# Performance work log

Measured on AMD Instinct MI355X. Metric: run time of the kernel, lower is better.

Reference implementation:

```python
import jax, jax.numpy as jnp
import numpy as np

N, IN_DIM, HID, Z, HEADS, E = 10000, 128, 128, 64, 4, 320000
NEG_SLOPE = 0.2


def setup_inputs() -> dict:
    key = jax.random.key(0)
    ks = jax.random.split(key, 16)
    s = 0.1
    return {
        "x": jax.random.normal(ks[0], (N, IN_DIM), jnp.float32),
        "edge_index": jax.random.randint(ks[1], (2, E), 0, N, jnp.int64),
        "gcn_w": jax.random.normal(ks[2], (IN_DIM, HID), jnp.float32) * s,
        "gcn_b": jnp.zeros((HID,), jnp.float32),
        "gat_w": jax.random.normal(ks[3], (HID, HEADS * HID), jnp.float32) * s,
        "gat_att_src": jax.random.normal(ks[4], (HEADS, HID), jnp.float32) * s,
        "gat_att_dst": jax.random.normal(ks[5], (HEADS, HID), jnp.float32) * s,
        "gat_b": jnp.zeros((HID,), jnp.float32),
        "mlp_w1": jax.random.normal(ks[6], (HID, HID), jnp.float32) * s,
        "mlp_b1": jnp.zeros((HID,), jnp.float32),
        "mlp_w2": jax.random.normal(ks[7], (HID, HID), jnp.float32) * s,
        "mlp_b2": jnp.zeros((HID,), jnp.float32),
        "mu_w": jax.random.normal(ks[8], (HID, Z), jnp.float32) * s,
        "mu_b": jnp.zeros((Z,), jnp.float32),
        "lv_w": jax.random.normal(ks[9], (HID, Z), jnp.float32) * s,
        "lv_b": jnp.zeros((Z,), jnp.float32),
    }


def _add_self_loops(edge_index, n):
    loop = jnp.arange(n, dtype=edge_index.dtype)
    src = jnp.concatenate([edge_index[0], loop])
    dst = jnp.concatenate([edge_index[1], loop])
    return src, dst


def _gcn(x, edge_index, w, b):
    # PyG GCNConv: add self-loops, symmetric normalization D^-1/2 (A+I) D^-1/2
    n = x.shape[0]
    src, dst = _add_self_loops(edge_index, n)
    deg = jax.ops.segment_sum(jnp.ones_like(dst, dtype=x.dtype), dst, num_segments=n)
    dinv = jax.lax.rsqrt(deg)  # deg >= 1 due to self-loops
    norm = dinv[src] * dinv[dst]  # [E+N]
    h = x @ w  # [N, HID]
    out = jax.ops.segment_sum(h[src] * norm[:, None], dst, num_segments=n)
    return out + b


def _gat(x, edge_index, w, att_src, att_dst, b):
    # PyG GATConv(heads=HEADS, concat=False): average heads, self-loops added
    n = x.shape[0]
    src, dst = _add_self_loops(edge_index, n)
    h = (x @ w).reshape(n, HEADS, HID)  # [N, H, C]
    a_src = jnp.einsum('nhc,hc->nh', h, att_src)  # [N, H]
    a_dst = jnp.einsum('nhc,hc->nh', h, att_dst)
    e = jax.nn.leaky_relu(a_src[src] + a_dst[dst], NEG_SLOPE)  # [E+N, H]
    # segment softmax over incoming edges of each destination node
    emax = jax.ops.segment_max(e, dst, num_segments=n)
    e = jnp.exp(e - emax[dst])
    denom = jax.ops.segment_sum(e, dst, num_segments=n)
    alpha = e / denom[dst]  # [E+N, H]
    out = jax.ops.segment_sum(h[src] * alpha[:, :, None], dst, num_segments=n)  # [N, H, C]
    return out.mean(axis=1) + b


def reference(x, edge_index, gcn_w, gcn_b, gat_w, gat_att_src, gat_att_dst, gat_b,
              mlp_w1, mlp_b1, mlp_w2, mlp_b2, mu_w, mu_b, lv_w, lv_b):
    h = jax.nn.relu(_gcn(x, edge_index, gcn_w, gcn_b))
    h = jax.nn.relu(_gat(h, edge_index, gat_w, gat_att_src, gat_att_dst, gat_b))
    h = jax.nn.relu(h @ mlp_w1 + mlp_b1)
    h = jax.nn.relu(h @ mlp_w2 + mlp_b2)
    mu = h @ mu_w + mu_b
    logvar = h @ lv_w + lv_b
    return (mu, logvar)
```

## Files before the change

### kernel.cpp

```cpp
#include <hip/hip_runtime.h>

#define NN 10000
#define D 128
#define NH 4
#define HD 512
#define ZD 64

__device__ __forceinline__ float lrelu(float x){ return x > 0.0f ? x : 0.2f*x; }

__global__ __launch_bounds__(256) void k_hist(const int* __restrict__ dst,
                                              int* __restrict__ deg, int E){
  int i = blockIdx.x*256 + threadIdx.x;
  if (i < E) atomicAdd(&deg[dst[i]], 1);
}

__global__ __launch_bounds__(1024) void k_scan(int* __restrict__ deg,
                                               int* __restrict__ ioff,
                                               float* __restrict__ dinv){
  __shared__ int part[1024];
  const int tid = threadIdx.x;
  const int base = tid*10;
  int local[10]; int s = 0;
#pragma unroll
  for (int i=0;i<10;i++){
    int idx = base+i;
    int v = (idx < NN) ? deg[idx] : 0;
    if (idx < NN) dinv[idx] = rsqrtf(1.0f + (float)v);
    local[i] = s; s += v;
  }
  part[tid] = s;
  __syncthreads();
  for (int o=1;o<1024;o<<=1){
    int v = (tid>=o) ? part[tid-o] : 0;
    __syncthreads();
    part[tid] += v;
    __syncthreads();
  }
  int excl = part[tid] - s;
#pragma unroll
  for (int i=0;i<10;i++){
    int idx = base+i;
    if (idx < NN){
      int o = excl + local[i];
      ioff[idx] = o;
      deg[idx]  = o;
    }
  }
  if (tid == 1023) ioff[NN] = part[1023];
}

__global__ __launch_bounds__(256) void k_fill(const int* __restrict__ src,
                                              const int* __restrict__ dst,
                                              int* __restrict__ cur,
                                              int* __restrict__ csr, int E,
                                              float* __restrict__ az){
  int i = blockIdx.x*256 + threadIdx.x;
  if (i < NN*NH*2) az[i] = 0.f;
  if (i >= E) return;
  int pos = atomicAdd(&cur[dst[i]], 1);
  csr[pos] = src[i];
}

__global__ __launch_bounds__(256) void k_mega(const float* __restrict__ x,
                                              const float* __restrict__ gcn_w,
                                              float* __restrict__ xw,
                                              const float* __restrict__ gat_w,
                                              const float* __restrict__ att_src,
                                              const float* __restrict__ att_dst,
                                              float* __restrict__ w_as,
                                              float* __restrict__ w_ad,
                                              int* __restrict__ icur){
  __shared__ float As[64][132];
  __shared__ float Ws[128][68];
  const int bx  = blockIdx.x;
  const int tid = threadIdx.x;
  if (bx < 314){
    const int row0 = (bx >> 1)*64;
    const int col0 = (bx & 1)*64;
#pragma unroll
    for (int i=0;i<8;i++){
      int f  = tid + i*256;
      int r  = f >> 5;
      int k4 = (f & 31) << 2;
      int rr = row0 + r;
      float4 v = make_float4(0.f,0.f,0.f,0.f);
      if (rr < NN) v = *(const float4*)&x[rr*D + k4];
      *(float4*)&As[r][k4] = v;
    }
#pragma unroll
    for (int i=0;i<8;i++){
      int f  = tid + i*256;
      int k  = f >> 4;
      int c4 = (f & 15) << 2;
      *(float4*)&Ws[k][c4] = *(const float4*)&gcn_w[k*D + col0 + c4];
    }
    __syncthreads();
    const int tx = tid & 15, ty = tid >> 4;
    float acc[4][4] = {{0.f}};
#pragma unroll 4
    for (int k=0;k<128;k++){
      float4 w = *(const float4*)&Ws[k][tx<<2];
      float wv[4] = {w.x, w.y, w.z, w.w};
      float av[4];
#pragma unroll
      for (int i=0;i<4;i++) av[i] = As[(ty<<2)+i][k];
#pragma unroll
      for (int i=0;i<4;i++)
#pragma unroll
        for (int j=0;j<4;j++) acc[i][j] = fmaf(av[i], wv[j], acc[i][j]);
    }
#pragma unroll
    for (int i=0;i<4;i++){
      int r = row0 + (ty<<2) + i;
      if (r >= NN) continue;
#pragma unroll
      for (int j=0;j<4;j++)
        xw[r*D + col0 + (tx<<2) + j] = acc[i][j];
    }
  } else if (bx < 318){
    const int h = bx - 314;
    const int k = tid;
    if (k < 128){
      const float* wrow = &gat_w[k*HD + h*D];
      const float* as   = &att_src[h*D];
      const float* ad   = &att_dst[h*D];
      float s = 0.f, d = 0.f;
#pragma unroll 4
      for (int c=0;c<D;c++){
        float wv = wrow[c];
        s = fmaf(wv, as[c], s);
        d = fmaf(wv, ad[c], d);
      }
      w_as[h*D + k] = s;
      w_ad[h*D + k] = d;
    }
  } else {
    int i = (bx - 318)*256 + tid;
    if (i < NN) icur[i] = 0;
  }
}

__global__ __launch_bounds__(256) void k_gcn_agg(const float* __restrict__ xw,
                                                 const float* __restrict__ dinv,
                                                 const int* __restrict__ ioff,
                                                 const int* __restrict__ csr,
                                                 const float* __restrict__ bias,
                                                 const float* __restrict__ w_as,
                                                 const float* __restrict__ w_ad,
                                                 float* __restrict__ out,
                                                 float* __restrict__ a_src,
                                                 float* __restrict__ a_dst){
  __shared__ float2 snm[4][64];
  const int sub  = blockIdx.x & 7;
  const int ch   = sub >> 2;
  const int g    = blockIdx.x >> 3;
  const int wv   = threadIdx.x >> 6;
  const int lane = threadIdx.x & 63;
  const int w    = g*16 + (sub & 3)*4 + wv;
  const int c    = ch*64 + lane;
  const int beg = ioff[w], end = ioff[w+1];
  float din = dinv[w];
  float ax = xw[w*D + c] * din;
  for (int jb = beg; jb < end; jb += 64){
    int cnt = end - jb; if (cnt > 64) cnt = 64;
    if (lane < cnt){
      int s = csr[jb + lane];
      snm[wv][lane] = make_float2(dinv[s], __int_as_float(s));
    }
    __builtin_amdgcn_wave_barrier();
#pragma unroll 4
    for (int l=0; l<cnt; l++){
      float2 t = snm[wv][l];
      int ss = __float_as_int(t.y);
      ax = fmaf(t.x, xw[ss*D + c], ax);
    }
    __builtin_amdgcn_wave_barrier();
  }
  float val = fmaxf(fmaf(ax, din, bias[c]), 0.f);
  out[w*D + c] = val;
  float ps[NH], pd[NH];
#pragma unroll
  for (int h=0;h<NH;h++){
    ps[h] = val * w_as[h*D + c];
    pd[h] = val * w_ad[h*D + c];
  }
#pragma unroll
  for (int o=32;o>0;o>>=1){
#pragma unroll
    for (int h=0;h<NH;h++){
      ps[h] += __shfl_xor(ps[h], o);
      pd[h] += __shfl_xor(pd[h], o);
    }
  }
  if (lane == 0){
#pragma unroll
    for (int h=0;h<NH;h++){
      atomicAdd(&a_src[w*4 + h], ps[h]);
      atomicAdd(&a_dst[w*4 + h], pd[h]);
    }
  }
}

__global__ __launch_bounds__(256) void k_gat_agg2(const float* __restrict__ h1,
                                                  const float* __restrict__ a_src,
                                                  const float* __restrict__ a_dst,
                                                  const int* __restrict__ ioff,
                                                  const int* __restrict__ csr,
                                                  float* __restrict__ agg){
  __shared__ float4 sal[4][64];
  __shared__ int    ssr[4][64];
  const int sub  = blockIdx.x & 7;
  const int ch   = sub >> 2;
  const int g    = blockIdx.x >> 3;
  const int wv   = threadIdx.x >> 6;
  const int lane = threadIdx.x & 63;
  const int w    = g*16 + (sub & 3)*4 + wv;
  const int c    = ch*64 + lane;
  const int beg = ioff[w], end = ioff[w+1];
  float4 ad  = *(const float4*)&a_dst[w*4];
  float4 asn = *(const float4*)&a_src[w*4];
  float e0 = __expf(lrelu(asn.x + ad.x));
  float e1 = __expf(lrelu(asn.y + ad.y));
  float e2 = __expf(lrelu(asn.z + ad.z));
  float e3 = __expf(lrelu(asn.w + ad.w));
  float hv = h1[w*D + c];
  float o0 = e0*hv, o1 = e1*hv, o2 = e2*hv, o3 = e3*hv;
  float den0=0.f, den1=0.f, den2=0.f, den3=0.f;

  for (int jb = beg; jb < end; jb += 64){
    int cnt = end - jb; if (cnt > 64) cnt = 64;
    if (lane < cnt){
      int s = csr[jb + lane];
      float4 as = *(const float4*)&a_src[s*4];
      float g0 = __expf(lrelu(as.x + ad.x));
      float g1 = __expf(lrelu(as.y + ad.y));
      float g2 = __expf(lrelu(as.z + ad.z));
      float g3 = __expf(lrelu(as.w + ad.w));
      sal[wv][lane] = make_float4(g0,g1,g2,g3);
      ssr[wv][lane] = s;
      den0 += g0; den1 += g1; den2 += g2; den3 += g3;
    }
    __builtin_amdgcn_wave_barrier();
#pragma unroll 4
    for (int l=0; l<cnt; l++){
      float4 b = sal[wv][l];
      float sv = h1[ssr[wv][l]*D + c];
      o0 = fmaf(b.x, sv, o0);
      o1 = fmaf(b.y, sv, o1);
      o2 = fmaf(b.z, sv, o2);
      o3 = fmaf(b.w, sv, o3);
    }
    __builtin_amdgcn_wave_barrier();
  }
#pragma unroll
  for (int o=32; o>0; o>>=1){
    den0 += __shfl_xor(den0, o);
    den1 += __shfl_xor(den1, o);
    den2 += __shfl_xor(den2, o);
    den3 += __shfl_xor(den3, o);
  }
  den0 += e0; den1 += e1; den2 += e2; den3 += e3;
  float* ab = &agg[(size_t)w*HD + c];
  ab[0*D] = o0 * (0.25f/den0);
  ab[1*D] = o1 * (0.25f/den1);
  ab[2*D] = o2 * (0.25f/den2);
  ab[3*D] = o3 * (0.25f/den3);
}

#define KLOOP(ACC)                                            \
  _Pragma("unroll 4")                                         \
  for (int k=0;k<128;k++){                                    \
    float4 wvv = *(const float4*)&Ws[k][tx<<2];               \
    float av = S[ty][k];                                      \
    ACC[0] = fmaf(av, wvv.x, ACC[0]);                         \
    ACC[1] = fmaf(av, wvv.y, ACC[1]);                         \
    ACC[2] = fmaf(av, wvv.z, ACC[2]);                         \
    ACC[3] = fmaf(av, wvv.w, ACC[3]);                         \
  }

__global__ __launch_bounds__(256) void k_gat_mlp(const float* __restrict__ agg,
                                                 const float* __restrict__ gat_w,
                                                 const float* __restrict__ gat_b,
                                                 const float* __restrict__ w1,
                                                 const float* __restrict__ b1,
                                                 const float* __restrict__ w2,
                                                 const float* __restrict__ b2,
                                                 const float* __restrict__ wmu,
                                                 const float* __restrict__ bmu,
                                                 const float* __restrict__ wlv,
                                                 const float* __restrict__ blv,
                                                 float* __restrict__ out){
  __shared__ float S[16][132];
  __shared__ float Ws[128][68];
  const int tid  = threadIdx.x;
  const int row0 = blockIdx.x*16;
  const int tx = tid & 15, ty = tid >> 4;
  float accA[4] = {0.f,0.f,0.f,0.f};
  float accB[4] = {0.f,0.f,0.f,0.f};

  for (int h=0; h<NH; h++){
    __syncthreads();
#pragma unroll
    for (int i=0;i<2;i++){
      int f  = tid + i*256;
      int r  = f >> 5;
      int k4 = (f & 31) << 2;
      *(float4*)&S[r][k4] = *(const float4*)&agg[(size_t)(row0+r)*HD + h*D + k4];
    }
    __syncthreads();
#pragma unroll
    for (int i=0;i<8;i++){
      int f  = tid + i*256;
      int k  = f >> 4;
      int c4 = (f & 15) << 2;
      *(float4*)&Ws[k][c4] = *(const float4*)&gat_w[k*HD + h*D + 0 + c4];
    }
    __syncthreads();
    KLOOP(accA)
    __syncthreads();
#pragma unroll
    for (int i=0;i<8;i++){
      int f  = tid + i*256;
      int k  = f >> 4;
      int c4 = (f & 15) << 2;
      *(float4*)&Ws[k][c4] = *(const float4*)&gat_w[k*HD + h*D + 64 + c4];
    }
    __syncthreads();
    KLOOP(accB)
  }
  __syncthreads();
#pragma unroll
  for (int j=0;j<4;j++){
    int c0 = (tx<<2) + j;
    S[ty][c0]      = fmaxf(accA[j] + gat_b[c0],      0.f);
    S[ty][c0 + 64] = fmaxf(accB[j] + gat_b[c0 + 64], 0.f);
  }

  for (int layer=0; layer<2; layer++){
    const float* W  = layer ? w2 : w1;
    const float* bb = layer ? b2 : b1;
#pragma unroll
    for (int j=0;j<4;j++){ accA[j] = 0.f; accB[j] = 0.f; }
    __syncthreads();
#pragma unroll
    for (int i=0;i<8;i++){
      int f  = tid + i*256;
      int k  = f >> 4;
      int c4 = (f & 15) << 2;
      *(float4*)&Ws[k][c4] = *(const float4*)&W[k*D + 0 + c4];
    }
    __syncthreads();
    KLOOP(accA)
    __syncthreads();
#pragma unroll
    for (int i=0;i<8;i++){
      int f  = tid + i*256;
      int k  = f >> 4;
      int c4 = (f & 15) << 2;
      *(float4*)&Ws[k][c4] = *(const float4*)&W[k*D + 64 + c4];
    }
    __syncthreads();
    KLOOP(accB)
    __syncthreads();
#pragma unroll
    for (int j=0;j<4;j++){
      int c0 = (tx<<2) + j;
      S[ty][c0]      = fmaxf(accA[j] + bb[c0],      0.f);
      S[ty][c0 + 64] = fmaxf(accB[j] + bb[c0 + 64], 0.f);
    }
  }

  for (int hd=0; hd<2; hd++){
    const float* W  = hd ? wlv : wmu;
    const float* bb = hd ? blv : bmu;
    float* ob = out + (size_t)hd*NN*ZD;
#pragma unroll
    for (int j=0;j<4;j++) accA[j] = 0.f;
    __syncthreads();
#pragma unroll
    for (int i=0;i<8;i++){
      int f  = tid + i*256;
      int k  = f >> 4;
      int c4 = (f & 15) << 2;
      *(float4*)&Ws[k][c4] = *(const float4*)&W[k*ZD + c4];
    }
    __syncthreads();
    KLOOP(accA)
    int r = row0 + ty;
    float4 v = make_float4(accA[0] + bb[(tx<<2)+0],
                           accA[1] + bb[(tx<<2)+1],
                           accA[2] + bb[(tx<<2)+2],
                           accA[3] + bb[(tx<<2)+3]);
    *(float4*)&ob[r*ZD + (tx<<2)] = v;
  }
}

extern "C" void kernel_launch(void* const* d_in, const int* in_sizes, int n_in,
                              void* d_out, int out_size, void* d_ws, size_t ws_size,
                              hipStream_t stream){
  const float* x     = (const float*)d_in[0];
  const int*   ei    = (const int*)d_in[1];
  const float* gcn_w = (const float*)d_in[2];
  const float* gcn_b = (const float*)d_in[3];
  const float* gat_w = (const float*)d_in[4];
  const float* att_s = (const float*)d_in[5];
  const float* att_d = (const float*)d_in[6];
  const float* gat_b = (const float*)d_in[7];
  const float* w1    = (const float*)d_in[8];
  const float* b1    = (const float*)d_in[9];
  const float* w2    = (const float*)d_in[10];
  const float* b2    = (const float*)d_in[11];
  const float* mu_w  = (const float*)d_in[12];
  const float* mu_b  = (const float*)d_in[13];
  const float* lv_w  = (const float*)d_in[14];
  const float* lv_b  = (const float*)d_in[15];
  const int E = in_sizes[1] / 2;
  const int* src = ei;
  const int* dst = ei + E;

  float* ws    = (float*)d_ws;
  float* xw    = ws;
  float* h1    = xw + NN*D;
  float* agg   = h1 + NN*D;
  float* dinv  = agg + (size_t)NN*HD;
  float* w_as  = dinv + NN;
  float* w_ad  = w_as + HD;
  float* a_src = w_ad + HD;
  float* a_dst = a_src + NN*NH;
  int*   ioff  = (int*)(a_dst + NN*NH);
  int*   icur  = ioff + NN + 1;
  int*   csr   = icur + NN;

  const int gE = (E + 255)/256;

  k_mega<<<358, 256, 0, stream>>>(x, gcn_w, xw, gat_w, att_s, att_d,
                                  w_as, w_ad, icur);
  k_hist<<<gE, 256, 0, stream>>>(dst, icur, E);
  k_scan<<<1, 1024, 0, stream>>>(icur, ioff, dinv);
  k_fill<<<gE, 256, 0, stream>>>(src, dst, icur, csr, E, a_src);

  k_gcn_agg<<<(NN/16)*8, 256, 0, stream>>>(xw, dinv, ioff, csr, gcn_b,
                                           w_as, w_ad, h1, a_src, a_dst);
  k_gat_agg2<<<(NN/16)*8, 256, 0, stream>>>(h1, a_src, a_dst, ioff, csr, agg);
  k_gat_mlp<<<NN/16, 256, 0, stream>>>(agg, gat_w, gat_b, w1, b1, w2, b2,
                                       mu_w, mu_b, lv_w, lv_b, (float*)d_out);
}
```

Measured before the change: 183.2 us.

## Use 4x4 register tiles and full-width weight tiles in fused GAT-MLP kernel

The fused GAT projection/MLP/head kernel now runs 128-thread blocks, and each thread computes a 4-row by 4-column output tile instead of a 1x4 strip. The weight tile in shared memory widens to all 128 columns, so each layer loads its weights once instead of in two 64-column halves, which removes barriers and passes. The mu and logvar heads are merged into a single 128-column pass. This raises arithmetic per shared-memory load, at the cost of fewer threads per block and a larger shared-memory footprint (about 76 KB), which may lower occupancy.

Result: slower. 242.0 us (+32.1%).

```diff
diff --git a/kernel.cpp b/kernel.cpp
--- a/kernel.cpp
+++ b/kernel.cpp
@@ -267,18 +267,25 @@
   ab[3*D] = o3 * (0.25f/den3);
 }
 
-#define KLOOP(ACC)                                            \
-  _Pragma("unroll 4")                                         \
-  for (int k=0;k<128;k++){                                    \
-    float4 wvv = *(const float4*)&Ws[k][tx<<2];               \
-    float av = S[ty][k];                                      \
-    ACC[0] = fmaf(av, wvv.x, ACC[0]);                         \
-    ACC[1] = fmaf(av, wvv.y, ACC[1]);                         \
-    ACC[2] = fmaf(av, wvv.z, ACC[2]);                         \
-    ACC[3] = fmaf(av, wvv.w, ACC[3]);                         \
-  }
-
-__global__ __launch_bounds__(256) void k_gat_mlp(const float* __restrict__ agg,
+#define KLOOP                                                   \
+  _Pragma("unroll 4")                                           \
+  for (int k=0;k<128;k++){                                      \
+    float4 wv = *(const float4*)&Ws[k][tx<<2];                  \
+    float a0 = S[(ty<<2)+0][k];                                 \
+    float a1 = S[(ty<<2)+1][k];                                 \
+    float a2 = S[(ty<<2)+2][k];                                 \
+    float a3 = S[(ty<<2)+3][k];                                 \
+    acc[0][0]=fmaf(a0,wv.x,acc[0][0]); acc[0][1]=fmaf(a0,wv.y,acc[0][1]); \
+    acc[0][2]=fmaf(a0,wv.z,acc[0][2]); acc[0][3]=fmaf(a0,wv.w,acc[0][3]); \
+    acc[1][0]=fmaf(a1,wv.x,acc[1][0]); acc[1][1]=fmaf(a1,wv.y,acc[1][1]); \
+    acc[1][2]=fmaf(a1,wv.z,acc[1][2]); acc[1][3]=fmaf(a1,wv.w,acc[1][3]); \
+    acc[2][0]=fmaf(a2,wv.x,acc[2][0]); acc[2][1]=fmaf(a2,wv.y,acc[2][1]); \
+    acc[2][2]=fmaf(a2,wv.z,acc[2][2]); acc[2][3]=fmaf(a2,wv.w,acc[2][3]); \
+    acc[3][0]=fmaf(a3,wv.x,acc[3][0]); acc[3][1]=fmaf(a3,wv.y,acc[3][1]); \
+    acc[3][2]=fmaf(a3,wv.z,acc[3][2]); acc[3][3]=fmaf(a3,wv.w,acc[3][3]); \
+  }
+
+__global__ __launch_bounds__(128) void k_gat_mlp(const float* __restrict__ agg,
                                                  const float* __restrict__ gat_w,
                                                  const float* __restrict__ gat_b,
                                                  const float* __restrict__ w1,
@@ -291,107 +298,91 @@
                                                  const float* __restrict__ blv,
                                                  float* __restrict__ out){
   __shared__ float S[16][132];
-  __shared__ float Ws[128][68];
+  __shared__ float Ws[128][132];
   const int tid  = threadIdx.x;
+  const int tx   = tid & 31;
+  const int ty   = tid >> 5;
   const int row0 = blockIdx.x*16;
-  const int tx = tid & 15, ty = tid >> 4;
-  float accA[4] = {0.f,0.f,0.f,0.f};
-  float accB[4] = {0.f,0.f,0.f,0.f};
+  float acc[4][4] = {{0.f}};
 
   for (int h=0; h<NH; h++){
     __syncthreads();
 #pragma unroll
-    for (int i=0;i<2;i++){
-      int f  = tid + i*256;
+    for (int i=0;i<4;i++){
+      int f  = tid + i*128;
       int r  = f >> 5;
       int k4 = (f & 31) << 2;
       *(float4*)&S[r][k4] = *(const float4*)&agg[(size_t)(row0+r)*HD + h*D + k4];
     }
-    __syncthreads();
-#pragma unroll
-    for (int i=0;i<8;i++){
-      int f  = tid + i*256;
-      int k  = f >> 4;
-      int c4 = (f & 15) << 2;
-      *(float4*)&Ws[k][c4] = *(const float4*)&gat_w[k*HD + h*D + 0 + c4];
-    }
-    __syncthreads();
-    KLOOP(accA)
-    __syncthreads();
-#pragma unroll
-    for (int i=0;i<8;i++){
-      int f  = tid + i*256;
-      int k  = f >> 4;
-      int c4 = (f & 15) << 2;
-      *(float4*)&Ws[k][c4] = *(const float4*)&gat_w[k*HD + h*D + 64 + c4];
-    }
-    __syncthreads();
-    KLOOP(accB)
+#pragma unroll
+    for (int i=0;i<32;i++){
+      int f  = tid + i*128;
+      int k  = f >> 5;
+      int c4 = (f & 31) << 2;
+      *(float4*)&Ws[k][c4] = *(const float4*)&gat_w[k*HD + h*D + c4];
+    }
+    __syncthreads();
+    KLOOP
   }
   __syncthreads();
 #pragma unroll
-  for (int j=0;j<4;j++){
-    int c0 = (tx<<2) + j;
-    S[ty][c0]      = fmaxf(accA[j] + gat_b[c0],      0.f);
-    S[ty][c0 + 64] = fmaxf(accB[j] + gat_b[c0 + 64], 0.f);
-  }
+  for (int i=0;i<4;i++)
+#pragma unroll
+    for (int j=0;j<4;j++){
+      int c = (tx<<2) + j;
+      S[(ty<<2)+i][c] = fmaxf(acc[i][j] + gat_b[c], 0.f);
+      acc[i][j] = 0.f;
+    }
 
   for (int layer=0; layer<2; layer++){
     const float* W  = layer ? w2 : w1;
     const float* bb = layer ? b2 : b1;
-#pragma unroll
-    for (int j=0;j<4;j++){ accA[j] = 0.f; accB[j] = 0.f; }
-    __syncthreads();
-#pragma unroll
-    for (int i=0;i<8;i++){
-      int f  = tid + i*256;
-      int k  = f >> 4;
-      int c4 = (f & 15) << 2;
-      *(float4*)&Ws[k][c4] = *(const float4*)&W[k*D + 0 + c4];
-    }
-    __syncthreads();
-    KLOOP(accA)
-    __syncthreads();
-#pragma unroll
-    for (int i=0;i<8;i++){
-      int f  = tid + i*256;
-      int k  = f >> 4;
-      int c4 = (f & 15) << 2;
-      *(float4*)&Ws[k][c4] = *(const float4*)&W[k*D + 64 + c4];
-    }
-    __syncthreads();
-    KLOOP(accB)
-    __syncthreads();
-#pragma unroll
-    for (int j=0;j<4;j++){
-      int c0 = (tx<<2) + j;
-      S[ty][c0]      = fmaxf(accA[j] + bb[c0],      0.f);
-      S[ty][c0 + 64] = fmaxf(accB[j] + bb[c0 + 64], 0.f);
-    }
-  }
-
-  for (int hd=0; hd<2; hd++){
-    const float* W  = hd ? wlv : wmu;
+    __syncthreads();
+#pragma unroll
+    for (int i=0;i<32;i++){
+      int f  = tid + i*128;
+      int k  = f >> 5;
+      int c4 = (f & 31) << 2;
+      *(float4*)&Ws[k][c4] = *(const float4*)&W[k*D + c4];
+    }
+    __syncthreads();
+    KLOOP
+    __syncthreads();
+#pragma unroll
+    for (int i=0;i<4;i++)
+#pragma unroll
+      for (int j=0;j<4;j++){
+        int c = (tx<<2) + j;
+        S[(ty<<2)+i][c] = fmaxf(acc[i][j] + bb[c], 0.f);
+        acc[i][j] = 0.f;
+      }
+  }
+
+  __syncthreads();
+#pragma unroll
+  for (int i=0;i<32;i++){
+    int f  = tid + i*128;
+    int k  = f >> 5;
+    int c4 = (f & 31) << 2;
+    const float* Wp = (c4 < ZD) ? &wmu[k*ZD + c4] : &wlv[k*ZD + (c4 - ZD)];
+    *(float4*)&Ws[k][c4] = *(const float4*)Wp;
+  }
+  __syncthreads();
+  KLOOP
+  {
+    const int hd = tx >> 4;
+    const int cl = (tx & 15) << 2;
     const float* bb = hd ? blv : bmu;
     float* ob = out + (size_t)hd*NN*ZD;
 #pragma unroll
-    for (int j=0;j<4;j++) accA[j] = 0.f;
-    __syncthreads();
-#pragma unroll
-    for (int i=0;i<8;i++){
-      int f  = tid + i*256;
-      int k  = f >> 4;
-      int c4 = (f & 15) << 2;
-      *(float4*)&Ws[k][c4] = *(const float4*)&W[k*ZD + c4];
-    }
-    __syncthreads();
-    KLOOP(accA)
-    int r = row0 + ty;
-    float4 v = make_float4(accA[0] + bb[(tx<<2)+0],
-                           accA[1] + bb[(tx<<2)+1],
-                           accA[2] + bb[(tx<<2)+2],
-                           accA[3] + bb[(tx<<2)+3]);
-    *(float4*)&ob[r*ZD + (tx<<2)] = v;
+    for (int i=0;i<4;i++){
+      int r = row0 + (ty<<2) + i;
+      float4 v = make_float4(acc[i][0] + bb[cl+0],
+                             acc[i][1] + bb[cl+1],
+                             acc[i][2] + bb[cl+2],
+                             acc[i][3] + bb[cl+3]);
+      *(float4*)&ob[r*ZD + cl] = v;
+    }
   }
 }
 
@@ -442,6 +433,6 @@
   k_gcn_agg<<<(NN/16)*8, 256, 0, stream>>>(xw, dinv, ioff, csr, gcn_b,
                                            w_as, w_ad, h1, a_src, a_dst);
   k_gat_agg2<<<(NN/16)*8, 256, 0, stream>>>(h1, a_src, a_dst, ioff, csr, agg);
-  k_gat_mlp<<<NN/16, 256, 0, stream>>>(agg, gat_w, gat_b, w1, b1, w2, b2,
+  k_gat_mlp<<<NN/16, 128, 0, stream>>>(agg, gat_w, gat_b, w1, b1, w2, b2,
                                        mu_w, mu_b, lv_w, lv_b, (float*)d_out);
 }
```
